# Kernel optimization log

Hardware: AMD Instinct MI355X
Metric: run time of the kernel (lower is better)

The kernel has to match this reference:

```python
import jax, jax.numpy as jnp
import numpy as np

HEADS = 4
DIM_QK = 128
SCALE = DIM_QK ** (-0.5)


def rel_to_abs(x):
    # x: [B, Nh, L, 2L-1] -> [B, Nh, L, L] via the skew trick
    B, Nh, L, _ = x.shape
    x = jnp.pad(x, ((0, 0), (0, 0), (0, 0), (0, 1)))          # [B,Nh,L,2L]
    flat = x.reshape(B, Nh, L * 2 * L)
    flat = jnp.pad(flat, ((0, 0), (0, 0), (0, L - 1)))
    final = flat.reshape(B, Nh, L + 1, 2 * L - 1)
    return final[:, :, :L, L - 1:]


def relative_logits_1d(q, rel_k):
    # q: [B, Nh, H, W, d], rel_k: [2W-1, d] -> [B, Nh, H, H, W, W] (axes b h x i y j)
    B, Nh, H, W, _ = q.shape
    rl = jnp.einsum('bnhwd,md->bnhwm', q, rel_k)              # [B,Nh,H,W,2W-1]
    rl = rl.reshape(B, Nh * H, W, 2 * W - 1)
    rl = rel_to_abs(rl)                                        # [B,Nh*H,W,W]
    rl = rl.reshape(B, Nh, H, W, W)
    rl = jnp.broadcast_to(rl[:, :, :, None, :, :], (B, Nh, H, H, W, W))
    return rl


def rel_pos_logits(q, rel_height, rel_width, H, W):
    # q: [B, h, HW, d]
    B, h, L, d = q.shape
    qg = q.reshape(B, h, H, W, d)
    # width direction: b h x i y j -> b h (x y) (i j)
    rw = relative_logits_1d(qg, rel_width)                     # [B,h,H,H,W,W]
    rw = rw.transpose(0, 1, 2, 4, 3, 5).reshape(B, h, H * W, H * W)
    # height direction: transpose x<->y, then b h x i y j -> b h (y x) (j i)
    qh = qg.transpose(0, 1, 3, 2, 4)                           # [B,h,W,H,d]
    rh = relative_logits_1d(qh, rel_height)                    # [B,h,W,W,H,H]
    rh = rh.transpose(0, 1, 4, 2, 5, 3).reshape(B, h, H * W, H * W)
    return rw + rh


def setup_inputs() -> dict:
    key = jax.random.key(0)
    ks = jax.random.split(key, 5)
    B, C, H, W = 16, 512, 32, 32
    scale = DIM_QK ** (-0.5)
    return {
        'featuremap': jax.random.normal(ks[0], (B, C, H, W), jnp.float32),
        'w_qk': jax.random.normal(ks[1], (2 * HEADS * DIM_QK, C), jnp.float32) * (C ** -0.5),
        'w_v': jax.random.normal(ks[2], (HEADS * 128, C), jnp.float32) * (C ** -0.5),
        'rel_height': jax.random.normal(ks[3], (2 * H - 1, DIM_QK), jnp.float32) * scale,
        'rel_width': jax.random.normal(ks[4], (2 * W - 1, DIM_QK), jnp.float32) * scale,
    }


def reference(featuremap, w_qk, w_v, rel_height, rel_width):
    B, C, H, W = featuremap.shape
    L = H * W
    # 1x1 conv projections (no bias) == channel matmuls
    qk = jnp.einsum('bchw,oc->bohw', featuremap, w_qk)         # [B, 2*h*dqk, H, W]
    v = jnp.einsum('bchw,oc->bohw', featuremap, w_v)           # [B, h*dv, H, W]
    q, k = jnp.split(qk, 2, axis=1)

    def to_heads(x):
        # B (h d) H W -> B h (H W) d
        d = x.shape[1] // HEADS
        return x.reshape(B, HEADS, d, L).transpose(0, 1, 3, 2)

    q, k, v = to_heads(q), to_heads(k), to_heads(v)
    q = q * SCALE
    logits = jnp.einsum('bhxd,bhyd->bhxy', q, k)
    logits = logits + rel_pos_logits(q, rel_height, rel_width, H, W)
    weights = jax.nn.softmax(logits, axis=-1)
    attn_out = jnp.einsum('bhxy,bhyd->bhxd', weights, v)       # [B,h,L,dv]
    dv = attn_out.shape[-1]
    # B h (H W) d -> B (h d) H W
    return attn_out.transpose(0, 1, 3, 2).reshape(B, HEADS * dv, H, W)
```

## Files before the change

kernel.cpp:

```cpp
#include <hip/hip_runtime.h>
#include <stdint.h>

typedef __attribute__((ext_vector_type(4))) float f32x4;
typedef __attribute__((ext_vector_type(16))) float f32x16;
typedef __attribute__((ext_vector_type(8))) short bf16x8;

#define DEV static __device__ __forceinline__

#define GLOAD16(g, l) __builtin_amdgcn_global_load_lds( \
    (const __attribute__((address_space(1))) void*)(g), \
    (__attribute__((address_space(3))) void*)(l), 16, 0, 0)

DEV unsigned short f2bf(float f){
  union { float f; uint32_t u; } v; v.f = f;
  return (unsigned short)((v.u + 0x7fffu + ((v.u >> 16) & 1u)) >> 16);
}

DEV uint32_t cvtpk(float a, float b){
  uint32_t r; asm("v_cvt_pk_bf16_f32 %0, %1, %2" : "=v"(r) : "v"(a), "v"(b)); return r;
}

DEV f32x4 mfma_bf16(bf16x8 a, bf16x8 b, f32x4 c){
  return __builtin_amdgcn_mfma_f32_16x16x32_bf16(a, b, c, 0, 0, 0);
}

DEV f32x16 mfma32(bf16x8 a, bf16x8 b, f32x16 c){
  return __builtin_amdgcn_mfma_f32_32x32x16_bf16(a, b, c, 0, 0, 0);
}

__global__ __launch_bounds__(256) void k_transpose_cvt(const float* __restrict__ fm,
                                                       unsigned short* __restrict__ xt){
  __shared__ float tile[64][65];
  int b = blockIdx.z, c0 = blockIdx.y * 64, l0 = blockIdx.x * 64;
  int t = threadIdx.x;
  int lr = t >> 4;
  int lc4 = (t & 15) * 4;
  const float* src = fm + ((size_t)b * 512 + c0) * 1024 + l0;
  #pragma unroll
  for (int i = 0; i < 4; i++){
    int r = lr + i * 16;
    f32x4 v = *(const f32x4*)&src[(size_t)r * 1024 + lc4];
    tile[r][lc4] = v[0]; tile[r][lc4 + 1] = v[1];
    tile[r][lc4 + 2] = v[2]; tile[r][lc4 + 3] = v[3];
  }
  __syncthreads();
  int j = t & 7;
  int lrow = t >> 3;
  unsigned short* dst = xt + ((size_t)b * 1024 + l0) * 512 + c0;
  #pragma unroll
  for (int i = 0; i < 2; i++){
    int l = lrow + i * 32;
    unsigned short tmp[8];
    #pragma unroll
    for (int u = 0; u < 8; u++) tmp[u] = f2bf(tile[j * 8 + u][l]);
    *(uint4*)&dst[(size_t)l * 512 + j * 8] = *(const uint4*)tmp;
  }
}

__global__ __launch_bounds__(256) void k_wcvt(const float* __restrict__ wqk,
                                              const float* __restrict__ wv,
                                              unsigned short* __restrict__ wb){
  int idx = blockIdx.x * 256 + threadIdx.x;
  int e = idx * 4;
  if (e >= 1536 * 512) return;
  const float* src = (e < 1024 * 512) ? (wqk + e) : (wv + (e - 1024 * 512));
  f32x4 v = *(const f32x4*)src;
  unsigned short* d = wb + e;
  d[0] = f2bf(v[0]); d[1] = f2bf(v[1]); d[2] = f2bf(v[2]); d[3] = f2bf(v[3]);
}

template<int MODE>
__global__ __launch_bounds__(256, 3) void k_proj(const unsigned short* __restrict__ Abase,
                                                 const unsigned short* __restrict__ Bbase,
                                                 unsigned short* __restrict__ qbuf,
                                                 unsigned short* __restrict__ kbuf,
                                                 unsigned short* __restrict__ vbuf){
  __shared__ unsigned short Al[128][64];
  __shared__ unsigned short Bl[128][64];
  int b = blockIdx.z;
  const unsigned short* A = Abase + (MODE == 0 ? (size_t)b * 1024 * 512 : 0);
  const unsigned short* B = Bbase + (MODE == 0 ? 0 : (size_t)b * 1024 * 512);
  int m0 = blockIdx.x * 128, n0 = blockIdx.y * 128;
  int t = threadIdx.x;
  int lane = t & 63, w = t >> 6;
  int wm = (w >> 1) * 64, wn = (w & 1) * 64;
  int l15 = lane & 15, lg = lane >> 4;
  int srow = lane >> 3;
  int scol = (lane & 7) * 8;
  f32x4 acc[4][4];
  for (int m = 0; m < 4; m++) for (int n = 0; n < 4; n++) acc[m][n] = (f32x4)(0.f);
  for (int k0 = 0; k0 < 512; k0 += 64){
    __syncthreads();
    #pragma unroll
    for (int i = 0; i < 4; i++){
      int j = w * 4 + i;
      GLOAD16(&A[(size_t)(m0 + j * 8 + srow) * 512 + k0 + scol], &Al[j * 8][0]);
      GLOAD16(&B[(size_t)(n0 + j * 8 + srow) * 512 + k0 + scol], &Bl[j * 8][0]);
    }
    __syncthreads();
    for (int dc = 0; dc < 2; dc++){
      bf16x8 af[4], bfr[4];
      for (int m = 0; m < 4; m++) af[m]  = *(const bf16x8*)&Al[wm + m * 16 + l15][dc * 32 + lg * 8];
      for (int n = 0; n < 4; n++) bfr[n] = *(const bf16x8*)&Bl[wn + n * 16 + l15][dc * 32 + lg * 8];
      for (int m = 0; m < 4; m++)
        for (int n = 0; n < 4; n++)
          acc[m][n] = mfma_bf16(af[m], bfr[n], acc[m][n]);
    }
  }
  for (int m = 0; m < 4; m++) for (int n = 0; n < 4; n++) for (int r = 0; r < 4; r++){
    int row = m0 + wm + m * 16 + lg * 4 + r;
    int col = n0 + wn + n * 16 + l15;
    float val = acc[m][n][r];
    if (MODE == 0){
      if (col < 512){
        int h = col >> 7, d = col & 127;
        qbuf[(((size_t)b * 4 + h) * 1024 + row) * 128 + d] = f2bf(val * 0.08838834764831845f);
      } else {
        int c2 = col - 512;
        int h = c2 >> 7, d = c2 & 127;
        kbuf[(((size_t)b * 4 + h) * 1024 + row) * 128 + d] = f2bf(val);
      }
    } else {
      vbuf[(((size_t)b * 4 + (row >> 7)) * 128 + (row & 127)) * 1024 + col] = f2bf(val);
    }
  }
}

__global__ __launch_bounds__(256, 2) void k_rel(const unsigned short* __restrict__ qbuf,
                                                const float* __restrict__ relh,
                                                const float* __restrict__ relw,
                                                float* __restrict__ Rel){
  int t = threadIdx.x;
  int lane = t & 63;
  int xi = blockIdx.x * 4 + (t >> 6);
  int bh = blockIdx.y;
  int mode = blockIdx.z;
  int l15 = lane & 15, lg = lane >> 4;
  const float* rel = (mode == 0) ? relh : relw;
  f32x4 acc[2][2];
  for (int m = 0; m < 2; m++) for (int n = 0; n < 2; n++) acc[m][n] = (f32x4)(0.f);
  for (int dc = 0; dc < 4; dc++){
    bf16x8 af[2], bb[2];
    for (int m = 0; m < 2; m++){
      int p = (mode == 0) ? (xi * 32 + m * 16 + l15) : ((m * 16 + l15) * 32 + xi);
      af[m] = *(const bf16x8*)&qbuf[((size_t)bh * 1024 + p) * 128 + dc * 32 + lg * 8];
    }
    for (int n = 0; n < 2; n++){
      int mrow = n * 16 + l15 - xi + 31;
      const float* rp = &rel[(size_t)mrow * 128 + dc * 32 + lg * 8];
      f32x4 r0 = *(const f32x4*)rp;
      f32x4 r1 = *(const f32x4*)(rp + 4);
      bf16x8 tt;
      for (int e = 0; e < 4; e++){ tt[e] = (short)f2bf(r0[e]); tt[e + 4] = (short)f2bf(r1[e]); }
      bb[n] = tt;
    }
    for (int m = 0; m < 2; m++)
      for (int n = 0; n < 2; n++)
        acc[m][n] = mfma_bf16(af[m], bb[n], acc[m][n]);
  }
  for (int m = 0; m < 2; m++) for (int n = 0; n < 2; n++) for (int r = 0; r < 4; r++){
    int a = m * 16 + lg * 4 + r;
    int outc = n * 16 + l15;
    int p = (mode == 0) ? (xi * 32 + a) : (a * 32 + xi);
    Rel[((size_t)bh * 1024 + p) * 64 + ((mode == 0) ? outc : 32 + outc)] = acc[m][n][r];
  }
}

__global__ __launch_bounds__(256, 2) void k_attn(const unsigned short* __restrict__ qbuf,
                                                 const unsigned short* __restrict__ kbuf,
                                                 const unsigned short* __restrict__ vbuf,
                                                 const float* __restrict__ Rel,
                                                 float* __restrict__ out){
  __shared__ unsigned short Kl[64 * 128];
  __shared__ unsigned short Vl[128 * 64];
  int bh = blockIdx.x;
  int q0 = blockIdx.y * 128;
  int t = threadIdx.x;
  int lane = t & 63, w = t >> 6;
  int l31 = lane & 31, hi = lane >> 5;
  int swz = (l31 & 7) * 8;
  int q = q0 + w * 32 + l31;
  const unsigned short* qg = qbuf + (size_t)bh * 1024 * 128;
  const unsigned short* kg = kbuf + (size_t)bh * 1024 * 128;
  const unsigned short* vg = vbuf + (size_t)bh * 128 * 1024;
  const float* relbh = Rel + (size_t)bh * 1024 * 64;

  bf16x8 qf[8];
  #pragma unroll
  for (int ks = 0; ks < 8; ks++)
    qf[ks] = *(const bf16x8*)&qg[(size_t)q * 128 + ks * 16 + hi * 8];

  float rwv[16];
  #pragma unroll
  for (int r = 0; r < 16; r++)
    rwv[r] = relbh[(size_t)q * 64 + 32 + (r & 3) + 8 * (r >> 2) + 4 * hi];

  bf16x8 ones;
  #pragma unroll
  for (int e = 0; e < 8; e++) ones[e] = (short)0x3F80;

  f32x16 o[4], osum;
  #pragma unroll
  for (int vb = 0; vb < 4; vb++) o[vb] = (f32x16)(0.f);
  osum = (f32x16)(0.f);

  bf16x8 kpre[4], vpre[4];
  #pragma unroll
  for (int i = 0; i < 4; i++){
    int c = t + i * 256;
    kpre[i] = *(const bf16x8*)&kg[(size_t)(c >> 4) * 128 + (c & 15) * 8];
    vpre[i] = *(const bf16x8*)&vg[(size_t)(c >> 3) * 1024 + (c & 7) * 8];
  }

  for (int kv0 = 0; kv0 < 1024; kv0 += 64){
    __syncthreads();
    #pragma unroll
    for (int i = 0; i < 4; i++){
      int c = t + i * 256;
      int kr = c >> 4;
      int vr = c >> 3;
      *(bf16x8*)&Kl[kr * 128 + (((c & 15) * 8) ^ ((kr & 7) * 8))] = kpre[i];
      *(bf16x8*)&Vl[vr * 64 + (((c & 7) * 8) ^ ((vr & 7) * 8))] = vpre[i];
    }
    __syncthreads();
    if (kv0 + 64 < 1024){
      int kvn = kv0 + 64;
      #pragma unroll
      for (int i = 0; i < 4; i++){
        int c = t + i * 256;
        kpre[i] = *(const bf16x8*)&kg[(size_t)(kvn + (c >> 4)) * 128 + (c & 15) * 8];
        vpre[i] = *(const bf16x8*)&vg[(size_t)(c >> 3) * 1024 + kvn + (c & 7) * 8];
      }
    }

    f32x16 s0 = (f32x16)(0.f), s1 = (f32x16)(0.f);
    __builtin_amdgcn_s_setprio(1);
    #pragma unroll
    for (int ks = 0; ks < 8; ks++){
      bf16x8 kf0 = *(const bf16x8*)&Kl[(size_t)l31 * 128 + ((ks * 16 + hi * 8) ^ swz)];
      bf16x8 kf1 = *(const bf16x8*)&Kl[(size_t)(32 + l31) * 128 + ((ks * 16 + hi * 8) ^ swz)];
      s0 = mfma32(kf0, qf[ks], s0);
      s1 = mfma32(kf1, qf[ks], s1);
    }
    __builtin_amdgcn_s_setprio(0);

    float rh0 = relbh[(size_t)q * 64 + (kv0 >> 5)];
    float rh1 = relbh[(size_t)q * 64 + (kv0 >> 5) + 1];

    float pb0[16], pb1[16];
    #pragma unroll
    for (int r = 0; r < 16; r++){
      pb0[r] = __expf(fminf(s0[r] + rh0 + rwv[r], 60.f));
      pb1[r] = __expf(fminf(s1[r] + rh1 + rwv[r], 60.f));
    }

    __builtin_amdgcn_s_setprio(1);
    #pragma unroll
    for (int kk = 0; kk < 4; kk++){
      const float* pb = (kk < 2) ? pb0 : pb1;
      int kkk = kk & 1;
      uint32_t c0 = cvtpk(pb[kkk * 8 + 0], pb[kkk * 8 + 1]);
      uint32_t c1 = cvtpk(pb[kkk * 8 + 2], pb[kkk * 8 + 3]);
      uint32_t c2 = cvtpk(pb[kkk * 8 + 4], pb[kkk * 8 + 5]);
      uint32_t c3 = cvtpk(pb[kkk * 8 + 6], pb[kkk * 8 + 7]);
      asm("v_permlane32_swap_b32 %0, %1" : "+v"(c0), "+v"(c2));
      asm("v_permlane32_swap_b32 %0, %1" : "+v"(c1), "+v"(c3));
      uint32_t words[4] = {c0, c1, c2, c3};
      bf16x8 pfrag = *(const bf16x8*)words;
      int vcol = kk * 16 + hi * 8;
      #pragma unroll
      for (int vb = 0; vb < 4; vb++){
        bf16x8 vf = *(const bf16x8*)&Vl[(size_t)(vb * 32 + l31) * 64 + (vcol ^ swz)];
        o[vb] = mfma32(vf, pfrag, o[vb]);
      }
      osum = mfma32(ones, pfrag, osum);
    }
    __builtin_amdgcn_s_setprio(0);
  }

  float inv = 1.f / osum[0];
  float* outb = out + (size_t)bh * 128 * 1024;
  #pragma unroll
  for (int vb = 0; vb < 4; vb++)
    #pragma unroll
    for (int r = 0; r < 16; r++){
      int dv = vb * 32 + (r & 3) + 8 * (r >> 2) + 4 * hi;
      outb[(size_t)dv * 1024 + q] = o[vb][r] * inv;
    }
}

extern "C" void kernel_launch(void* const* d_in, const int* in_sizes, int n_in,
                              void* d_out, int out_size, void* d_ws, size_t ws_size,
                              hipStream_t stream){
  const float* fm   = (const float*)d_in[0];
  const float* wqk  = (const float*)d_in[1];
  const float* wv   = (const float*)d_in[2];
  const float* relh = (const float*)d_in[3];
  const float* relw = (const float*)d_in[4];
  float* out = (float*)d_out;
  char* ws = (char*)d_ws;
  if (ws_size < (size_t)68681728) return;

  unsigned short* qb = (unsigned short*)(ws);
  unsigned short* kb = (unsigned short*)(ws + ((size_t)16 << 20));
  unsigned short* vb = (unsigned short*)(ws + ((size_t)32 << 20));
  unsigned short* xt = (unsigned short*)(ws + ((size_t)48 << 20));
  float* Rel         = (float*)(ws + ((size_t)48 << 20));
  unsigned short* wb = (unsigned short*)(ws + ((size_t)64 << 20));

  hipLaunchKernelGGL(k_transpose_cvt, dim3(16, 8, 16), dim3(256), 0, stream, fm, xt);
  hipLaunchKernelGGL(k_wcvt, dim3(768), dim3(256), 0, stream, wqk, wv, wb);
  hipLaunchKernelGGL(k_proj<0>, dim3(8, 8, 16), dim3(256), 0, stream, xt, wb, qb, kb, vb);
  hipLaunchKernelGGL(k_proj<1>, dim3(4, 8, 16), dim3(256), 0, stream,
                     wb + (size_t)1024 * 512, xt, qb, kb, vb);
  hipLaunchKernelGGL(k_rel, dim3(8, 64, 2), dim3(256), 0, stream, qb, relh, relw, Rel);
  hipLaunchKernelGGL(k_attn, dim3(64, 8), dim3(256), 0, stream, qb, kb, vb, Rel, out);
}
```

Baseline: 119.6 us.

## Split KV range across two wave groups per attention block and combine partials

New measurement: 312.4 us. 161% more time.

```diff
diff --git a/kernel.cpp b/kernel.cpp
--- a/kernel.cpp
+++ b/kernel.cpp
@@ -166,24 +166,29 @@
   }
 }
 
-__global__ __launch_bounds__(256, 2) void k_attn(const unsigned short* __restrict__ qbuf,
+__global__ __launch_bounds__(512, 4) void k_attn(const unsigned short* __restrict__ qbuf,
                                                  const unsigned short* __restrict__ kbuf,
                                                  const unsigned short* __restrict__ vbuf,
                                                  const float* __restrict__ Rel,
                                                  float* __restrict__ out){
-  __shared__ unsigned short Kl[64 * 128];
-  __shared__ unsigned short Vl[128 * 64];
+  __shared__ unsigned short stage[2][16384];
+  __shared__ float cmbsum[4][64];
   int bh = blockIdx.x;
   int q0 = blockIdx.y * 128;
   int t = threadIdx.x;
   int lane = t & 63, w = t >> 6;
+  int wq = w & 3, grp = w >> 2;
+  int tg = t & 255;
   int l31 = lane & 31, hi = lane >> 5;
   int swz = (l31 & 7) * 8;
-  int q = q0 + w * 32 + l31;
+  int q = q0 + wq * 32 + l31;
+  int kvb = grp * 512;
   const unsigned short* qg = qbuf + (size_t)bh * 1024 * 128;
   const unsigned short* kg = kbuf + (size_t)bh * 1024 * 128;
   const unsigned short* vg = vbuf + (size_t)bh * 128 * 1024;
   const float* relbh = Rel + (size_t)bh * 1024 * 64;
+  unsigned short* Kl = &stage[grp][0];
+  unsigned short* Vl = &stage[grp][8192];
 
   bf16x8 qf[8];
   #pragma unroll
@@ -207,27 +212,27 @@
   bf16x8 kpre[4], vpre[4];
   #pragma unroll
   for (int i = 0; i < 4; i++){
-    int c = t + i * 256;
-    kpre[i] = *(const bf16x8*)&kg[(size_t)(c >> 4) * 128 + (c & 15) * 8];
-    vpre[i] = *(const bf16x8*)&vg[(size_t)(c >> 3) * 1024 + (c & 7) * 8];
-  }
-
-  for (int kv0 = 0; kv0 < 1024; kv0 += 64){
+    int c = tg + i * 256;
+    kpre[i] = *(const bf16x8*)&kg[(size_t)(kvb + (c >> 4)) * 128 + (c & 15) * 8];
+    vpre[i] = *(const bf16x8*)&vg[(size_t)(c >> 3) * 1024 + kvb + (c & 7) * 8];
+  }
+
+  for (int kv0 = 0; kv0 < 512; kv0 += 64){
     __syncthreads();
     #pragma unroll
     for (int i = 0; i < 4; i++){
-      int c = t + i * 256;
+      int c = tg + i * 256;
       int kr = c >> 4;
       int vr = c >> 3;
       *(bf16x8*)&Kl[kr * 128 + (((c & 15) * 8) ^ ((kr & 7) * 8))] = kpre[i];
       *(bf16x8*)&Vl[vr * 64 + (((c & 7) * 8) ^ ((vr & 7) * 8))] = vpre[i];
     }
     __syncthreads();
-    if (kv0 + 64 < 1024){
-      int kvn = kv0 + 64;
+    if (kv0 + 64 < 512){
+      int kvn = kvb + kv0 + 64;
       #pragma unroll
       for (int i = 0; i < 4; i++){
-        int c = t + i * 256;
+        int c = tg + i * 256;
         kpre[i] = *(const bf16x8*)&kg[(size_t)(kvn + (c >> 4)) * 128 + (c & 15) * 8];
         vpre[i] = *(const bf16x8*)&vg[(size_t)(c >> 3) * 1024 + kvn + (c & 7) * 8];
       }
@@ -244,8 +249,9 @@
     }
     __builtin_amdgcn_s_setprio(0);
 
-    float rh0 = relbh[(size_t)q * 64 + (kv0 >> 5)];
-    float rh1 = relbh[(size_t)q * 64 + (kv0 >> 5) + 1];
+    int y0 = (kvb + kv0) >> 5;
+    float rh0 = relbh[(size_t)q * 64 + y0];
+    float rh1 = relbh[(size_t)q * 64 + y0 + 1];
 
     float pb0[16], pb1[16];
     #pragma unroll
@@ -278,15 +284,37 @@
     __builtin_amdgcn_s_setprio(0);
   }
 
-  float inv = 1.f / osum[0];
-  float* outb = out + (size_t)bh * 128 * 1024;
-  #pragma unroll
-  for (int vb = 0; vb < 4; vb++)
-    #pragma unroll
-    for (int r = 0; r < 16; r++){
-      int dv = vb * 32 + (r & 3) + 8 * (r >> 2) + 4 * hi;
-      outb[(size_t)dv * 1024 + q] = o[vb][r] * inv;
-    }
+  __syncthreads();
+  f32x4* cmb = (f32x4*)&stage[0][0];
+  if (grp == 1){
+    #pragma unroll
+    for (int vb = 0; vb < 4; vb++)
+      #pragma unroll
+      for (int rq = 0; rq < 4; rq++){
+        f32x4 v;
+        v[0] = o[vb][rq * 4 + 0]; v[1] = o[vb][rq * 4 + 1];
+        v[2] = o[vb][rq * 4 + 2]; v[3] = o[vb][rq * 4 + 3];
+        cmb[((vb * 4 + rq) * 4 + wq) * 64 + lane] = v;
+      }
+    cmbsum[wq][lane] = osum[0];
+  }
+  __syncthreads();
+  if (grp == 0){
+    float inv = 1.f / (osum[0] + cmbsum[wq][lane]);
+    float* outb = out + (size_t)bh * 128 * 1024;
+    #pragma unroll
+    for (int vb = 0; vb < 4; vb++)
+      #pragma unroll
+      for (int rq = 0; rq < 4; rq++){
+        f32x4 vB = cmb[((vb * 4 + rq) * 4 + wq) * 64 + lane];
+        #pragma unroll
+        for (int j = 0; j < 4; j++){
+          int r = rq * 4 + j;
+          int dv = vb * 32 + (r & 3) + 8 * (r >> 2) + 4 * hi;
+          outb[(size_t)dv * 1024 + q] = (o[vb][r] + vB[j]) * inv;
+        }
+      }
+  }
 }
 
 extern "C" void kernel_launch(void* const* d_in, const int* in_sizes, int n_in,
@@ -314,5 +342,5 @@
   hipLaunchKernelGGL(k_proj<1>, dim3(4, 8, 16), dim3(256), 0, stream,
                      wb + (size_t)1024 * 512, xt, qb, kb, vb);
   hipLaunchKernelGGL(k_rel, dim3(8, 64, 2), dim3(256), 0, stream, qb, relh, relw, Rel);
-  hipLaunchKernelGGL(k_attn, dim3(64, 8), dim3(256), 0, stream, qb, kb, vb, Rel, out);
-}
+  hipLaunchKernelGGL(k_attn, dim3(64, 8), dim3(512), 0, stream, qb, kb, vb, Rel, out);
+}
```
